# Performance work log

Hardware: AMD Instinct MI355X
Metric: run time of the kernel (lower is better)

Reference implementation:

```python
import jax, jax.numpy as jnp
import numpy as np


def rotary_pos_emb(x):
    # x: [..., seq, dim], dim even. Interleaved (GPT-NeoX-style pairwise) rotary.
    dim, seq = x.shape[-1], x.shape[-2]
    ts = jnp.arange(0, dim, 2, dtype=jnp.float32)
    inv_freqs = 10000.0 ** (-ts / dim)
    grid = jnp.arange(seq, dtype=jnp.float32)[:, None] * inv_freqs[None, :]  # [s, dim//2]
    sin = jnp.repeat(jnp.sin(grid), 2, axis=-1).astype(x.dtype)  # [s, dim]
    cos = jnp.repeat(jnp.cos(grid), 2, axis=-1).astype(x.dtype)  # [s, dim]
    x1, x2 = x[..., ::2], x[..., 1::2]
    xs = jnp.stack([-x2, x1], axis=-1).reshape(x.shape)  # interleave (-x2, x1)
    return x * cos + xs * sin


def setup_inputs() -> dict:
    key = jax.random.key(0)
    kx, kq, kk, kv, ko = jax.random.split(key, 5)
    B, S, D = 2, 2048, 1024
    scale = 1.0 / np.sqrt(D)
    x = jax.random.normal(kx, (B, S, D), dtype=jnp.float32)
    mask = jnp.tril(jnp.ones((S, S), dtype=bool))  # causal
    Wq = jax.random.normal(kq, (D, D), dtype=jnp.float32) * scale
    Wk = jax.random.normal(kk, (D, D), dtype=jnp.float32) * scale
    Wv = jax.random.normal(kv, (D, D), dtype=jnp.float32) * scale
    Wo = jax.random.normal(ko, (D, D), dtype=jnp.float32) * scale
    return {"x": x, "mask": mask, "Wq": Wq, "Wk": Wk, "Wv": Wv, "Wo": Wo}


def reference(x, mask, Wq, Wk, Wv, Wo):
    H = 16
    POS_PORTION = 0.5
    B, S, D = x.shape
    K = D // H
    p = int(K * POS_PORTION)

    q = (x @ Wq) / (K ** 0.5)
    q = q.reshape(B, S, H, K).transpose(0, 2, 1, 3)  # b h l k
    q = jnp.concatenate([rotary_pos_emb(q[..., :p]), q[..., p:]], axis=-1)

    k = (x @ Wk).reshape(B, S, H, K).transpose(0, 2, 1, 3)
    k = jnp.concatenate([rotary_pos_emb(k[..., :p]), k[..., p:]], axis=-1)

    v = (x @ Wv).reshape(B, S, H, K).transpose(0, 2, 1, 3)

    logits = jnp.einsum('bhik,bhjk->bhij', q, k)
    # full-precision masked softmax
    l32 = logits.astype(jnp.float32)
    l32 = jnp.where(mask, l32, -1e30)
    a = jax.nn.softmax(l32, axis=-1).astype(logits.dtype)

    y = jnp.einsum('bhij,bhjv->bhiv', a, v)
    y = y.transpose(0, 2, 1, 3).reshape(B, S, D)  # b l (h v)
    return y @ Wo
```

## Files before the change

kernel.cpp:

```cpp
#include <hip/hip_runtime.h>
#include <cstdint>
#include <cstddef>

typedef __bf16 bf16;
typedef __bf16 bf16x8 __attribute__((ext_vector_type(8)));
typedef float  f32x4  __attribute__((ext_vector_type(4)));
typedef short  s16x4  __attribute__((ext_vector_type(4)));

#define B_  2
#define S_  2048
#define D_  1024
#define H_  16
#define KH  64

__device__ __forceinline__ void gload_lds16(const bf16* gp, bf16* lds_base) {
    __builtin_amdgcn_global_load_lds(
        (const __attribute__((address_space(1))) unsigned int*)gp,
        (__attribute__((address_space(3))) unsigned int*)lds_base,
        16, 0, 0);
}

__global__ __launch_bounds__(256) void prep(
    const float* __restrict__ x, bf16* __restrict__ xb,
    const float* __restrict__ Wq, const float* __restrict__ Wk,
    const float* __restrict__ Wv, const float* __restrict__ Wo,
    bf16* __restrict__ WqkvT, bf16* __restrict__ WoT)
{
    __shared__ bf16 tl[64][72];
    int z = blockIdx.x;
    if (z < 4096) {
        const int i = (z * 256 + threadIdx.x) * 4;
        const float4 v = *(const float4*)(x + i);
        union { int2 w; bf16 e[4]; } u;
        u.e[0] = (bf16)v.x; u.e[1] = (bf16)v.y;
        u.e[2] = (bf16)v.z; u.e[3] = (bf16)v.w;
        *(int2*)(xb + i) = u.w;
        return;
    }
    z -= 4096;
    const int zx = z & 15, zy = (z >> 4) & 15, zw = z >> 8;
    const float* src = (zw == 0) ? Wq : (zw == 1) ? Wk : (zw == 2) ? Wv : Wo;
    bf16* dst = (zw < 3) ? (WqkvT + (size_t)zw * D_ * D_) : WoT;
    const int r0 = zy * 64;
    const int c0 = zx * 64;
    const int t  = threadIdx.x;
    {
        const int r = t >> 2, cs = (t & 3) * 16;
        const float4* p = (const float4*)(src + (size_t)(r0 + r) * D_ + c0 + cs);
        float4 a0 = p[0], a1 = p[1], a2 = p[2], a3 = p[3];
        tl[cs +  0][r] = (bf16)a0.x; tl[cs +  1][r] = (bf16)a0.y;
        tl[cs +  2][r] = (bf16)a0.z; tl[cs +  3][r] = (bf16)a0.w;
        tl[cs +  4][r] = (bf16)a1.x; tl[cs +  5][r] = (bf16)a1.y;
        tl[cs +  6][r] = (bf16)a1.z; tl[cs +  7][r] = (bf16)a1.w;
        tl[cs +  8][r] = (bf16)a2.x; tl[cs +  9][r] = (bf16)a2.y;
        tl[cs + 10][r] = (bf16)a2.z; tl[cs + 11][r] = (bf16)a2.w;
        tl[cs + 12][r] = (bf16)a3.x; tl[cs + 13][r] = (bf16)a3.y;
        tl[cs + 14][r] = (bf16)a3.z; tl[cs + 15][r] = (bf16)a3.w;
    }
    __syncthreads();
    {
        const int c = t >> 2, rs = (t & 3) * 16;
        union { int4 v[2]; bf16 e[16]; } u;
#pragma unroll
        for (int i = 0; i < 16; ++i) u.e[i] = tl[c][rs + i];
        int4* p = (int4*)(dst + (size_t)(c0 + c) * D_ + r0 + rs);
        p[0] = u.v[0]; p[1] = u.v[1];
    }
}

template <int EPI, int BN>
__global__ __launch_bounds__(256, BN == 96 ? 4 : 2) void gemm_bt(
    const bf16* __restrict__ A, const bf16* __restrict__ BT,
    float* __restrict__ C, int N, int Kd,
    bf16* __restrict__ qp, bf16* __restrict__ kp, bf16* __restrict__ vp)
{
    constexpr int NJF = BN / 32;
    __shared__ bf16 As[128 * 64];
    __shared__ bf16 Bs[BN * 64];
    const int tid  = threadIdx.x;
    const int lane = tid & 63;
    const int wave = tid >> 6;
    const int l15  = lane & 15;
    const int quad = lane >> 4;
    const int m0 = blockIdx.y * 128;
    const int n0 = blockIdx.x * BN;
    const int wm = (wave >> 1) * 64;
    const int wn = (wave & 1) * (BN / 2);

    const int srow = lane >> 3;
    const int sg   = (lane & 7) ^ srow;

    f32x4 acc[4][NJF];
#pragma unroll
    for (int i = 0; i < 4; ++i)
#pragma unroll
        for (int j = 0; j < NJF; ++j) acc[i][j] = f32x4{0.f, 0.f, 0.f, 0.f};

    for (int k0 = 0; k0 < Kd; k0 += 64) {
        __syncthreads();
#pragma unroll
        for (int c = 0; c < 4; ++c) {
            const int r0 = wave * 32 + c * 8;
            gload_lds16(A + (size_t)(m0 + r0 + srow) * Kd + k0 + sg * 8,
                        As + r0 * 64);
        }
#pragma unroll
        for (int c = 0; c < NJF; ++c) {
            const int r0 = wave * (BN / 4) + c * 8;
            gload_lds16(BT + (size_t)(n0 + r0 + srow) * Kd + k0 + sg * 8,
                        Bs + r0 * 64);
        }
        __syncthreads();
#pragma unroll
        for (int c = 0; c < 2; ++c) {
            bf16x8 af[4], bfv[NJF];
#pragma unroll
            for (int i = 0; i < 4; ++i)
                af[i] = *(const bf16x8*)
                    &As[(wm + i * 16 + l15) * 64 + (((c * 4 + quad) ^ (l15 & 7)) * 8)];
#pragma unroll
            for (int j = 0; j < NJF; ++j)
                bfv[j] = *(const bf16x8*)
                    &Bs[(wn + j * 16 + l15) * 64 + (((c * 4 + quad) ^ (l15 & 7)) * 8)];
#pragma unroll
            for (int i = 0; i < 4; ++i)
#pragma unroll
                for (int j = 0; j < NJF; ++j)
                    acc[i][j] = __builtin_amdgcn_mfma_f32_16x16x32_bf16(
                        af[i], bfv[j], acc[i][j], 0, 0, 0);
        }
    }

#pragma unroll
    for (int i = 0; i < 4; ++i)
#pragma unroll
        for (int j = 0; j < NJF; ++j) {
            const int Rb = m0 + wm + i * 16 + quad * 4;
            const int Cc = n0 + wn + j * 16 + l15;
            if (EPI == 0) {
#pragma unroll
                for (int r = 0; r < 4; ++r)
                    C[(size_t)(Rb + r) * N + Cc] = acc[i][j][r];
            } else {
                const int sec = Cc >> 10, cc = Cc & 1023;
                const int h = cc >> 6, kd = cc & 63;
                if (sec == 2) {
                    const int b = Rb >> 11, s0 = Rb & (S_ - 1);
                    union { s16x4 sv; bf16 e[4]; } pv;
#pragma unroll
                    for (int r = 0; r < 4; ++r) pv.e[r] = (bf16)acc[i][j][r];
                    *(s16x4*)&vp[((size_t)(b * H_ + h) * KH + kd) * S_ + s0] = pv.sv;
                } else {
#pragma unroll
                    for (int r = 0; r < 4; ++r) {
                        const int row = Rb + r;
                        const int b = row >> 11, s = row & (S_ - 1);
                        float v = acc[i][j][r];
                        if (sec == 0) {
                            qp[((size_t)(b * H_ + h) * S_ + s) * KH + kd] =
                                (bf16)(v * 0.1803368801111204f);
                        } else {
                            if ((kd >> 4) < 2) {
                                const float partner = __shfl_xor(v, 1);
                                const float inv = __builtin_exp2f(
                                    -(float)(kd >> 1) * (13.28771237954945f / 16.f));
                                const float ang = (float)s * inv;
                                float sn, cn;
                                __sincosf(ang, &sn, &cn);
                                v = (l15 & 1) ? fmaf(partner, sn, v * cn)
                                              : fmaf(-partner, sn, v * cn);
                            }
                            kp[((size_t)(b * H_ + h) * S_ + s) * KH + kd] = (bf16)v;
                        }
                    }
                }
            }
        }
}

__global__ __launch_bounds__(256, 4) void attn(
    const bf16* __restrict__ q, const bf16* __restrict__ k,
    const bf16* __restrict__ vt, bf16* __restrict__ y)
{
    __shared__ bf16 Ks[2][64 * 64];
    __shared__ bf16 VTs[2][64 * 64];

    const int z  = blockIdx.x;
    const int g  = z & 7;
    const int u  = (z >> 3) & 31;
    const int w  = z >> 8;
    const int bh = g + ((u >> 3) << 3);
    const int v_ = u & 7;
    const int qt = (w == 0) ? v_ : (w == 1) ? (15 - v_)
                 : (w == 2) ? (16 + v_) : (31 - v_);
    const int b  = bh >> 4, h = bh & 15;
    const int t    = threadIdx.x;
    const int lane = t & 63, wave = t >> 6;
    const int l15  = lane & 15, quad = lane >> 4;
    const int wq   = wave >> 1;
    const int wk   = wave & 1;
    const int q0   = qt * 64 + wq * 32;

    const bf16* kbh = k  + (size_t)bh * S_ * KH;
    const bf16* vbh = vt + (size_t)bh * KH * S_;

    const int srow = lane >> 3;
    const int sg   = (lane & 7) ^ srow;

    auto stage = [&](int jt, int bb) {
        const int j0 = jt * 64;
#pragma unroll
        for (int i = 0; i < 2; ++i) {
            const int c = wave * 2 + i;
            gload_lds16(kbh + (size_t)(j0 + c * 8 + srow) * KH + sg * 8,
                        &Ks[bb][c * 8 * 64]);
            gload_lds16(vbh + (size_t)(c * 8 + srow) * S_ + j0 + sg * 8,
                        &VTs[bb][c * 8 * 64]);
        }
    };

    s16x4 ones4;
#pragma unroll
    for (int i = 0; i < 4; ++i) ones4[i] = (short)0x3F80;

    float* red = (wq == 0) ? (float*)&Ks[0][0] : (float*)&VTs[0][0];

    bf16x8 qf[2][2];
#pragma unroll
    for (int qb = 0; qb < 2; ++qb) {
        const bf16* qptr = q + ((size_t)bh * S_ + q0 + qb * 16 + l15) * KH + quad * 8;
        qf[qb][0] = *(const bf16x8*)qptr;
        qf[qb][1] = *(const bf16x8*)(qptr + 32);
        const float s = (float)(q0 + qb * 16 + l15);
#pragma unroll
        for (int tt = 0; tt < 4; ++tt) {
            const int i = quad * 4 + tt;
            const float inv = exp2f(-(float)i * (13.28771237954945f / 16.f));
            const float ang = s * inv;
            const float sn = sinf(ang), cn = cosf(ang);
            const float x0 = (float)qf[qb][0][2 * tt], x1 = (float)qf[qb][0][2 * tt + 1];
            qf[qb][0][2 * tt]     = (bf16)(x0 * cn - x1 * sn);
            qf[qb][0][2 * tt + 1] = (bf16)(x1 * cn + x0 * sn);
        }
    }

    f32x4 accO[2][4], lacc[2];
#pragma unroll
    for (int qb = 0; qb < 2; ++qb) {
#pragma unroll
        for (int vb = 0; vb < 4; ++vb) accO[qb][vb] = f32x4{0.f, 0.f, 0.f, 0.f};
        lacc[qb] = f32x4{0.f, 0.f, 0.f, 0.f};
    }

    const int nj = qt + 1;
    stage(0, 0);
    for (int jt = 0; jt < nj; ++jt) {
        const int bb = jt & 1;
        __syncthreads();
        if (jt + 1 < nj) stage(jt + 1, bb ^ 1);

        f32x4 accS[2][2];
#pragma unroll
        for (int kb = 0; kb < 2; ++kb)
#pragma unroll
            for (int qb = 0; qb < 2; ++qb) accS[kb][qb] = f32x4{0.f, 0.f, 0.f, 0.f};
#pragma unroll
        for (int c = 0; c < 2; ++c) {
            bf16x8 kf[2];
#pragma unroll
            for (int kb = 0; kb < 2; ++kb)
                kf[kb] = *(const bf16x8*)
                    &Ks[bb][(wk * 32 + kb * 16 + l15) * 64 +
                            (((c * 4 + quad) ^ (l15 & 7)) * 8)];
            __builtin_amdgcn_s_setprio(1);
#pragma unroll
            for (int kb = 0; kb < 2; ++kb)
#pragma unroll
                for (int qb = 0; qb < 2; ++qb)
                    accS[kb][qb] = __builtin_amdgcn_mfma_f32_16x16x32_bf16(
                        kf[kb], qf[qb][c], accS[kb][qb], 0, 0, 0);
            __builtin_amdgcn_s_setprio(0);
        }

        if (jt == nj - 1) {
            const int j0 = jt * 64;
#pragma unroll
            for (int kb = 0; kb < 2; ++kb)
#pragma unroll
                for (int qb = 0; qb < 2; ++qb) {
                    const int qi = q0 + qb * 16 + l15;
#pragma unroll
                    for (int r = 0; r < 4; ++r) {
                        const int ki = j0 + wk * 32 + kb * 16 + quad * 4 + r;
                        if (ki > qi) accS[kb][qb][r] = -1e30f;
                    }
                }
        }

        s16x4 pf[2][2];
#pragma unroll
        for (int kb = 0; kb < 2; ++kb)
#pragma unroll
            for (int qb = 0; qb < 2; ++qb) {
                union { bf16 hh[4]; s16x4 ss; } u2;
#pragma unroll
                for (int r = 0; r < 4; ++r)
                    u2.hh[r] = (bf16)__builtin_amdgcn_exp2f(accS[kb][qb][r]);
                pf[kb][qb] = u2.ss;
            }

#pragma unroll
        for (int kb = 0; kb < 2; ++kb) {
            s16x4 vf[4];
#pragma unroll
            for (int vb = 0; vb < 4; ++vb)
                vf[vb] = *(const s16x4*)
                    &VTs[bb][(vb * 16 + l15) * 64 +
                             (((wk * 4 + kb * 2 + (quad >> 1)) ^ (l15 & 7)) * 8) +
                             (quad & 1) * 4];
            __builtin_amdgcn_s_setprio(1);
#pragma unroll
            for (int qb = 0; qb < 2; ++qb) {
#pragma unroll
                for (int vb = 0; vb < 4; ++vb)
                    accO[qb][vb] = __builtin_amdgcn_mfma_f32_16x16x16bf16_1k(
                        pf[kb][qb], vf[vb], accO[qb][vb], 0, 0, 0);
                lacc[qb] = __builtin_amdgcn_mfma_f32_16x16x16bf16_1k(
                    pf[kb][qb], ones4, lacc[qb], 0, 0, 0);
            }
            __builtin_amdgcn_s_setprio(0);
        }
    }

    __syncthreads();
    if (wk == 1) {
#pragma unroll
        for (int qb = 0; qb < 2; ++qb) {
#pragma unroll
            for (int vb = 0; vb < 4; ++vb)
#pragma unroll
                for (int r = 0; r < 4; ++r)
                    red[(((qb * 4 + vb) * 4) + r) * 64 + lane] = accO[qb][vb][r];
#pragma unroll
            for (int r = 0; r < 4; ++r)
                red[(32 + qb * 4 + r) * 64 + lane] = lacc[qb][r];
        }
    }
    __syncthreads();
    if (wk == 0) {
#pragma unroll
        for (int qb = 0; qb < 2; ++qb) {
            float rinv[4];
#pragma unroll
            for (int r = 0; r < 4; ++r)
                rinv[r] = 1.0f / (lacc[qb][r] + red[(32 + qb * 4 + r) * 64 + lane]);
#pragma unroll
            for (int vb = 0; vb < 4; ++vb)
#pragma unroll
                for (int r = 0; r < 4; ++r) {
                    const float o = accO[qb][vb][r] +
                                    red[(((qb * 4 + vb) * 4) + r) * 64 + lane];
                    const int row = q0 + qb * 16 + quad * 4 + r;
                    const int col = h * KH + vb * 16 + l15;
                    y[((size_t)b * S_ + row) * D_ + col] = (bf16)(o * rinv[r]);
                }
        }
    }
}

extern "C" void kernel_launch(void* const* d_in, const int* in_sizes, int n_in,
                              void* d_out, int out_size, void* d_ws, size_t ws_size,
                              hipStream_t stream)
{
    (void)in_sizes; (void)n_in; (void)out_size; (void)ws_size;
    const float* x  = (const float*)d_in[0];
    const float* Wq = (const float*)d_in[2];
    const float* Wk = (const float*)d_in[3];
    const float* Wv = (const float*)d_in[4];
    const float* Wo = (const float*)d_in[5];
    float* out = (float*)d_out;

    char* ws = (char*)d_ws;
    bf16* WqkvT = (bf16*)(ws + 0);
    bf16* WoT   = (bf16*)(ws + 6291456);
    bf16* xb    = (bf16*)(ws + 8388608);
    bf16* qw    = (bf16*)(ws + 16777216);
    bf16* kw    = (bf16*)(ws + 25165824);
    bf16* vtw   = (bf16*)(ws + 33554432);
    bf16* yw    = (bf16*)(ws + 41943040);

    hipLaunchKernelGGL(prep, dim3(5120), dim3(256), 0, stream,
                       x, xb, Wq, Wk, Wv, Wo, WqkvT, WoT);
    hipLaunchKernelGGL((gemm_bt<1, 96>), dim3(32, 32), dim3(256), 0, stream,
                       xb, WqkvT, (float*)nullptr, 3072, 1024, qw, kw, vtw);
    hipLaunchKernelGGL(attn, dim3(1024), dim3(256), 0, stream, qw, kw, vtw, yw);
    hipLaunchKernelGGL((gemm_bt<0, 64>), dim3(16, 32), dim3(256), 0, stream,
                       yw, WoT, out, 1024, 1024,
                       (bf16*)nullptr, (bf16*)nullptr, (bf16*)nullptr);
}
```

Before: 183.7 us.

## Load K and V fragments directly from global memory instead of LDS staging

The attention kernel drops its double-buffered LDS staging of K and V tiles and the per-iteration block barrier. Each wave now reads its MFMA fragments straight from global memory, relying on L1/L2 caching, and LDS is kept only for the final cross-wave reduction. This removes the barrier and LDS traffic, but waves sharing a tile now load it redundantly and global-load latency is exposed with no prefetch.

```diff
diff --git a/kernel.cpp b/kernel.cpp
--- a/kernel.cpp
+++ b/kernel.cpp
@@ -182,8 +182,7 @@
     const bf16* __restrict__ q, const bf16* __restrict__ k,
     const bf16* __restrict__ vt, bf16* __restrict__ y)
 {
-    __shared__ bf16 Ks[2][64 * 64];
-    __shared__ bf16 VTs[2][64 * 64];
+    __shared__ float red[2][40 * 64];
 
     const int z  = blockIdx.x;
     const int g  = z & 7;
@@ -204,26 +203,12 @@
     const bf16* kbh = k  + (size_t)bh * S_ * KH;
     const bf16* vbh = vt + (size_t)bh * KH * S_;
 
-    const int srow = lane >> 3;
-    const int sg   = (lane & 7) ^ srow;
-
-    auto stage = [&](int jt, int bb) {
-        const int j0 = jt * 64;
-#pragma unroll
-        for (int i = 0; i < 2; ++i) {
-            const int c = wave * 2 + i;
-            gload_lds16(kbh + (size_t)(j0 + c * 8 + srow) * KH + sg * 8,
-                        &Ks[bb][c * 8 * 64]);
-            gload_lds16(vbh + (size_t)(c * 8 + srow) * S_ + j0 + sg * 8,
-                        &VTs[bb][c * 8 * 64]);
-        }
-    };
+    const bf16* kf_base = kbh + (size_t)(wk * 32 + l15) * KH + quad * 8;
+    const bf16* vf_base = vbh + (size_t)l15 * S_ + wk * 32 + quad * 4;
 
     s16x4 ones4;
 #pragma unroll
     for (int i = 0; i < 4; ++i) ones4[i] = (short)0x3F80;
-
-    float* red = (wq == 0) ? (float*)&Ks[0][0] : (float*)&VTs[0][0];
 
     bf16x8 qf[2][2];
 #pragma unroll
@@ -252,38 +237,34 @@
         lacc[qb] = f32x4{0.f, 0.f, 0.f, 0.f};
     }
 
-    const int nj = qt + 1;
-    stage(0, 0);
-    for (int jt = 0; jt < nj; ++jt) {
-        const int bb = jt & 1;
-        __syncthreads();
-        if (jt + 1 < nj) stage(jt + 1, bb ^ 1);
+    for (int jt = 0; jt <= qt; ++jt) {
+        const int j0 = jt * 64;
+
+        bf16x8 kf[2][2];
+#pragma unroll
+        for (int c = 0; c < 2; ++c)
+#pragma unroll
+            for (int kb = 0; kb < 2; ++kb)
+                kf[c][kb] = *(const bf16x8*)
+                    (kf_base + (size_t)(j0 + kb * 16) * KH + c * 32);
 
         f32x4 accS[2][2];
 #pragma unroll
         for (int kb = 0; kb < 2; ++kb)
 #pragma unroll
             for (int qb = 0; qb < 2; ++qb) accS[kb][qb] = f32x4{0.f, 0.f, 0.f, 0.f};
-#pragma unroll
-        for (int c = 0; c < 2; ++c) {
-            bf16x8 kf[2];
-#pragma unroll
-            for (int kb = 0; kb < 2; ++kb)
-                kf[kb] = *(const bf16x8*)
-                    &Ks[bb][(wk * 32 + kb * 16 + l15) * 64 +
-                            (((c * 4 + quad) ^ (l15 & 7)) * 8)];
-            __builtin_amdgcn_s_setprio(1);
+        __builtin_amdgcn_s_setprio(1);
+#pragma unroll
+        for (int c = 0; c < 2; ++c)
 #pragma unroll
             for (int kb = 0; kb < 2; ++kb)
 #pragma unroll
                 for (int qb = 0; qb < 2; ++qb)
                     accS[kb][qb] = __builtin_amdgcn_mfma_f32_16x16x32_bf16(
-                        kf[kb], qf[qb][c], accS[kb][qb], 0, 0, 0);
-            __builtin_amdgcn_s_setprio(0);
-        }
-
-        if (jt == nj - 1) {
-            const int j0 = jt * 64;
+                        kf[c][kb], qf[qb][c], accS[kb][qb], 0, 0, 0);
+        __builtin_amdgcn_s_setprio(0);
+
+        if (jt == qt) {
 #pragma unroll
             for (int kb = 0; kb < 2; ++kb)
 #pragma unroll
@@ -315,9 +296,7 @@
 #pragma unroll
             for (int vb = 0; vb < 4; ++vb)
                 vf[vb] = *(const s16x4*)
-                    &VTs[bb][(vb * 16 + l15) * 64 +
-                             (((wk * 4 + kb * 2 + (quad >> 1)) ^ (l15 & 7)) * 8) +
-                             (quad & 1) * 4];
+                    (vf_base + (size_t)(vb * 16) * S_ + j0 + kb * 16);
             __builtin_amdgcn_s_setprio(1);
 #pragma unroll
             for (int qb = 0; qb < 2; ++qb) {
@@ -340,10 +319,10 @@
             for (int vb = 0; vb < 4; ++vb)
 #pragma unroll
                 for (int r = 0; r < 4; ++r)
-                    red[(((qb * 4 + vb) * 4) + r) * 64 + lane] = accO[qb][vb][r];
+                    red[wq][(((qb * 4 + vb) * 4) + r) * 64 + lane] = accO[qb][vb][r];
 #pragma unroll
             for (int r = 0; r < 4; ++r)
-                red[(32 + qb * 4 + r) * 64 + lane] = lacc[qb][r];
+                red[wq][(32 + qb * 4 + r) * 64 + lane] = lacc[qb][r];
         }
     }
     __syncthreads();
@@ -353,13 +332,13 @@
             float rinv[4];
 #pragma unroll
             for (int r = 0; r < 4; ++r)
-                rinv[r] = 1.0f / (lacc[qb][r] + red[(32 + qb * 4 + r) * 64 + lane]);
+                rinv[r] = 1.0f / (lacc[qb][r] + red[wq][(32 + qb * 4 + r) * 64 + lane]);
 #pragma unroll
             for (int vb = 0; vb < 4; ++vb)
 #pragma unroll
                 for (int r = 0; r < 4; ++r) {
                     const float o = accO[qb][vb][r] +
-                                    red[(((qb * 4 + vb) * 4) + r) * 64 + lane];
+                                    red[wq][(((qb * 4 + vb) * 4) + r) * 64 + lane];
                     const int row = q0 + qb * 16 + quad * 4 + r;
                     const int col = h * KH + vb * 16 + l15;
                     y[((size_t)b * S_ + row) * D_ + col] = (bf16)(o * rinv[r]);
```

Result: slower. 243.0 us (+32.3%).
